# Optimization experiments

Hardware: AMD Instinct MI355X
Metric: run time of the kernel (lower is better)

## Reference

```python
import jax, jax.numpy as jnp
import numpy as np

KNN = 10        # knn init arg
FAC = 2.0       # fac init arg
SIGMA = 0.5     # self.sigma (fixed in module)
N, D = 4096, 128


def setup_inputs() -> dict:
    key = jax.random.key(0)
    k1, k2, k3 = jax.random.split(key, 3)
    return {
        "x": jax.random.normal(k1, (N, D), dtype=jnp.float32),
        "alpha": 0.01 * jax.random.normal(k2, (D,), dtype=jnp.float32),
        "base_noise": jax.random.normal(k3, (D,), dtype=jnp.float32),
    }


def _full_affinity_knn(Xm):
    r = jnp.sum(Xm * Xm, axis=1, keepdims=True)          # [N,1]
    Dx = r - 2.0 * (Xm @ Xm.T) + r.T                     # [N,N]
    # full row sort, take (knn-1)-th smallest distance per row
    sorted_d = jnp.sort(Dx, axis=1)                      # [N,N]
    knn_d = sorted_d[:, KNN - 1]                         # [N]
    # calculate_percentiles(percentile=50)
    s = jnp.sort(knn_d)
    n = s.shape[0]
    idx = int(50.0 / 100.0 * n)
    if n % 2 == 0:
        mu, ml = s[idx], s[idx - 1]
    else:
        mu = ml = s[idx]
    sigma = (mu + ml) / 2.0
    sigma = jnp.where(sigma < 1e-8, jnp.float32(1.0), sigma)
    W = jnp.exp(-Dx / (FAC * sigma))                     # [N,N]
    # Dminus @ W == row-normalize (diag matmul replaced by broadcast divide)
    P = W / jnp.sum(W, axis=1, keepdims=True)
    return P


def reference(x, alpha, base_noise):
    # feature_selector: hard_sigmoid(alpha + sigma*noise) applied per-feature
    z = alpha + SIGMA * base_noise
    gate = jnp.clip(z + 0.5, 0.0, 1.0)
    masked = x * gate[None, :]                           # [N,D]
    P = _full_affinity_knn(masked)                       # [N,N]
    return (P, masked)
```

## Files before the change

### kernel.cpp

```cpp
#include <hip/hip_runtime.h>
#include <math.h>

#define NROW 4096
#define NDIM 128
#define KNN 10
#define LDSS 136

typedef __bf16 bf16x8 __attribute__((ext_vector_type(8)));
typedef unsigned short u16x8 __attribute__((ext_vector_type(8)));
typedef float f32x4 __attribute__((ext_vector_type(4)));

__device__ inline unsigned short f2bf(float f) {
    unsigned int u = __float_as_uint(f);
    u += 0x7FFFu + ((u >> 16) & 1u);
    return (unsigned short)(u >> 16);
}
__device__ inline float bf2f(unsigned short u) {
    return __uint_as_float((unsigned)u << 16);
}


__global__ __launch_bounds__(128) void k_mask(const float* __restrict__ x,
                                              const float* __restrict__ alpha,
                                              const float* __restrict__ noise,
                                              float* __restrict__ masked,
                                              float* __restrict__ r) {
    int row = blockIdx.x;
    int c = threadIdx.x;
    float g = alpha[c] + 0.5f * noise[c] + 0.5f;
    g = fminf(fmaxf(g, 0.0f), 1.0f);
    float m = x[row * NDIM + c] * g;
    masked[row * NDIM + c] = m;
    float v = m * m;
#pragma unroll
    for (int o = 32; o > 0; o >>= 1) v += __shfl_down(v, o, 64);
    __shared__ float partial[2];
    if ((c & 63) == 0) partial[c >> 6] = v;
    __syncthreads();
    if (c == 0) r[row] = partial[0] + partial[1];
}

__global__ __launch_bounds__(256) void k_dx(const float* __restrict__ M,
                                            const float* __restrict__ r,
                                            float* __restrict__ P) {
    __shared__ __align__(16) __bf16 Asm[128 * LDSS];
    __shared__ __align__(16) __bf16 Bsm[128 * LDSS];
    int tid = threadIdx.x;
    int bx = blockIdx.x, by = blockIdx.y;

    {
        const float* Ap = M + (size_t)by * 128 * NDIM;
        const float* Bp = M + (size_t)bx * 128 * NDIM;
        int c = (tid & 15) * 8;
        int r0 = tid >> 4;
#pragma unroll
        for (int i = 0; i < 8; ++i) {
            int row = r0 + i * 16;
            float4 a0 = *(const float4*)(Ap + row * NDIM + c);
            float4 a1 = *(const float4*)(Ap + row * NDIM + c + 4);
            uint4 pa;
            pa.x = (unsigned)f2bf(a0.x) | ((unsigned)f2bf(a0.y) << 16);
            pa.y = (unsigned)f2bf(a0.z) | ((unsigned)f2bf(a0.w) << 16);
            pa.z = (unsigned)f2bf(a1.x) | ((unsigned)f2bf(a1.y) << 16);
            pa.w = (unsigned)f2bf(a1.z) | ((unsigned)f2bf(a1.w) << 16);
            *(uint4*)&Asm[row * LDSS + c] = pa;
            float4 b0 = *(const float4*)(Bp + row * NDIM + c);
            float4 b1 = *(const float4*)(Bp + row * NDIM + c + 4);
            uint4 pb;
            pb.x = (unsigned)f2bf(b0.x) | ((unsigned)f2bf(b0.y) << 16);
            pb.y = (unsigned)f2bf(b0.z) | ((unsigned)f2bf(b0.w) << 16);
            pb.z = (unsigned)f2bf(b1.x) | ((unsigned)f2bf(b1.y) << 16);
            pb.w = (unsigned)f2bf(b1.z) | ((unsigned)f2bf(b1.w) << 16);
            *(uint4*)&Bsm[row * LDSS + c] = pb;
        }
    }
    __syncthreads();

    int wave = tid >> 6, lane = tid & 63;
    int wr = wave >> 1, wc = wave & 1;
    int quad = lane >> 4, l15 = lane & 15;

    f32x4 acc[4][4];
#pragma unroll
    for (int i = 0; i < 4; ++i)
#pragma unroll
        for (int j = 0; j < 4; ++j) acc[i][j] = (f32x4)(0.0f);

#pragma unroll
    for (int kk = 0; kk < 128; kk += 32) {
        int ka = kk + quad * 8;
        bf16x8 af[4], bfr[4];
#pragma unroll
        for (int ti = 0; ti < 4; ++ti)
            af[ti] = *(const bf16x8*)&Asm[(wr * 64 + ti * 16 + l15) * LDSS + ka];
#pragma unroll
        for (int tj = 0; tj < 4; ++tj)
            bfr[tj] = *(const bf16x8*)&Bsm[(wc * 64 + tj * 16 + l15) * LDSS + ka];
#pragma unroll
        for (int ti = 0; ti < 4; ++ti)
#pragma unroll
            for (int tj = 0; tj < 4; ++tj)
                acc[ti][tj] = __builtin_amdgcn_mfma_f32_16x16x32_bf16(
                    af[ti], bfr[tj], acc[ti][tj], 0, 0, 0);
    }

    int gi_base = by * 128 + wr * 64;
    int gj_base = bx * 128 + wc * 64;
    float rrow[4][4], rcol[4];
#pragma unroll
    for (int ti = 0; ti < 4; ++ti)
#pragma unroll
        for (int rg = 0; rg < 4; ++rg)
            rrow[ti][rg] = r[gi_base + ti * 16 + quad * 4 + rg];
#pragma unroll
    for (int tj = 0; tj < 4; ++tj) rcol[tj] = r[gj_base + tj * 16 + l15];
#pragma unroll
    for (int ti = 0; ti < 4; ++ti)
#pragma unroll
        for (int rg = 0; rg < 4; ++rg) {
            int grow = gi_base + ti * 16 + quad * 4 + rg;
            __bf16* brow = (__bf16*)(P + (size_t)grow * NROW + NROW / 2);
#pragma unroll
            for (int tj = 0; tj < 4; ++tj) {
                int gcol = gj_base + tj * 16 + l15;
                float d = rrow[ti][rg] + rcol[tj] - 2.0f * acc[ti][tj][rg];
                ((unsigned short*)brow)[gcol] = f2bf(d);
            }
        }
}

__global__ __launch_bounds__(256) void k_knn(const float* __restrict__ P,
                                             float* __restrict__ knn) {
    int tid = threadIdx.x;
    int wave = tid >> 6, lane = tid & 63;
    int row = blockIdx.x * 4 + wave;
    const unsigned short* drow =
        (const unsigned short*)(P + (size_t)row * NROW + NROW / 2);

    float t[KNN];
#pragma unroll
    for (int j = 0; j < KNN; ++j) t[j] = INFINITY;

#pragma unroll
    for (int c = 0; c < 8; ++c) {
        u16x8 v8 = *(const u16x8*)(drow + (c * 64 + lane) * 8);
#pragma unroll
        for (int e = 0; e < 8; ++e) {
            float cv = bf2f(v8[e]);
#pragma unroll
            for (int j = 0; j < KNN; ++j) {
                float lo = fminf(t[j], cv);
                cv = fmaxf(t[j], cv);
                t[j] = lo;
            }
        }
    }

#pragma unroll
    for (int r = 0; r < KNN; ++r) {
        float v = t[0];
        int src = lane;
#pragma unroll
        for (int o = 1; o < 64; o <<= 1) {
            float ov = __shfl_xor(v, o, 64);
            int osrc = __shfl_xor(src, o, 64);
            if (ov < v || (ov == v && osrc < src)) { v = ov; src = osrc; }
        }
        if (r == KNN - 1) {
            if (lane == 0) knn[row] = v;
        } else if (src == lane) {
#pragma unroll
            for (int j = 0; j < KNN - 1; ++j) t[j] = t[j + 1];
            t[KNN - 1] = INFINITY;
        }
    }
}

__device__ inline unsigned fmap(float f) {
    unsigned b = __float_as_uint(f);
    return b ^ ((b >> 31) ? 0xFFFFFFFFu : 0x80000000u);
}
__device__ inline float funmap(unsigned u) {
    unsigned b = (u & 0x80000000u) ? (u ^ 0x80000000u) : ~u;
    return __uint_as_float(b);
}

__global__ __launch_bounds__(1024) void k_sigma(const float* __restrict__ knn,
                                                float* __restrict__ scale_out) {
    __shared__ unsigned keys[NROW];
    __shared__ unsigned hist[2048];
    __shared__ unsigned s_prefix, s_R;
    __shared__ float red_f[16];
    __shared__ unsigned red_u[16];
    int tid = threadIdx.x;
    if (tid == 0) { s_prefix = 0; s_R = 2047; }
#pragma unroll
    for (int l = 0; l < 4; ++l) keys[tid + l * 1024] = fmap(knn[tid + l * 1024]);
    __syncthreads();

    const int shifts[3] = {21, 10, 0};
    const int widths[3] = {11, 11, 10};
    for (int rd = 0; rd < 3; ++rd) {
        int sh = shifts[rd], w = widths[rd];
        unsigned nb = 1u << w;
        hist[tid] = 0;
        hist[tid + 1024] = 0;
        __syncthreads();
        unsigned prefix = s_prefix;
        unsigned R = s_R;
        int hsh = sh + w;
#pragma unroll
        for (int l = 0; l < 4; ++l) {
            unsigned k = keys[tid + l * 1024];
            bool match = (rd == 0) || ((k >> hsh) == prefix);
            if (match) atomicAdd(&hist[(k >> sh) & (nb - 1u)], 1u);
        }
        __syncthreads();
        if (tid < 64) {
            unsigned chunk = nb >> 6;
            unsigned base = tid * chunk;
            unsigned lsum = 0;
            for (unsigned i = 0; i < chunk; ++i) lsum += hist[base + i];
            unsigned pfx = lsum;
#pragma unroll
            for (int o = 1; o < 64; o <<= 1) {
                unsigned v = __shfl_up(pfx, o, 64);
                if (tid >= o) pfx += v;
            }
            unsigned excl = pfx - lsum;
            if (R >= excl && R < excl + lsum) {
                unsigned cum = excl;
                for (unsigned i = 0; i < chunk; ++i) {
                    unsigned h = hist[base + i];
                    if (R < cum + h) {
                        s_prefix = (prefix << w) | (base + i);
                        s_R = R - cum;
                        break;
                    }
                    cum += h;
                }
            }
        }
        __syncthreads();
    }

    unsigned mlk = s_prefix;
    unsigned cnt = 0, mng = 0xFFFFFFFFu;
#pragma unroll
    for (int l = 0; l < 4; ++l) {
        unsigned k = keys[tid + l * 1024];
        if (k <= mlk) cnt++;
        else mng = min(mng, k);
    }
#pragma unroll
    for (int o = 32; o > 0; o >>= 1) {
        cnt += __shfl_down(cnt, o, 64);
        mng = min(mng, (unsigned)__shfl_down(mng, o, 64));
    }
    int lane = tid & 63, wid = tid >> 6;
    if (lane == 0) { red_u[wid] = cnt; red_f[wid] = __uint_as_float(mng); }
    __syncthreads();
    if (tid == 0) {
        unsigned ctot = 0, m = 0xFFFFFFFFu;
        for (int w = 0; w < 16; ++w) {
            ctot += red_u[w];
            m = min(m, __float_as_uint(red_f[w]));
        }
        float ml = funmap(mlk);
        float mu = (ctot >= 2049u) ? ml : funmap(m);
        float sigma = 0.5f * (mu + ml);
        if (sigma < 1e-8f) sigma = 1.0f;
        scale_out[0] = -1.0f / (2.0f * sigma);
    }
}

__global__ __launch_bounds__(256) void k_norm(float* __restrict__ P,
                                              const float* __restrict__ scale_p) {
    int row = blockIdx.x, tid = threadIdx.x;
    float scale = scale_p[0];
    float* drow = P + (size_t)row * NROW;
    const unsigned short* brow = (const unsigned short*)(drow + NROW / 2);

    u16x8 a = *(const u16x8*)(brow + tid * 16);
    u16x8 b = *(const u16x8*)(brow + tid * 16 + 8);
    float v[16];
#pragma unroll
    for (int e = 0; e < 8; ++e) v[e] = __expf(bf2f(a[e]) * scale);
#pragma unroll
    for (int e = 0; e < 8; ++e) v[8 + e] = __expf(bf2f(b[e]) * scale);
    float sum = 0.0f;
#pragma unroll
    for (int e = 0; e < 16; ++e) sum += v[e];
#pragma unroll
    for (int o = 32; o > 0; o >>= 1) sum += __shfl_down(sum, o, 64);
    __shared__ float ps[4];
    int lane = tid & 63, wid = tid >> 6;
    if (lane == 0) ps[wid] = sum;
    __syncthreads();
    float inv = 1.0f / (ps[0] + ps[1] + ps[2] + ps[3]);
#pragma unroll
    for (int l = 0; l < 4; ++l) {
        float4 o4;
        o4.x = v[l * 4 + 0] * inv;
        o4.y = v[l * 4 + 1] * inv;
        o4.z = v[l * 4 + 2] * inv;
        o4.w = v[l * 4 + 3] * inv;
        *(float4*)(drow + tid * 16 + l * 4) = o4;
    }
}

extern "C" void kernel_launch(void* const* d_in, const int* in_sizes, int n_in,
                              void* d_out, int out_size, void* d_ws, size_t ws_size,
                              hipStream_t stream) {
    const float* x = (const float*)d_in[0];
    const float* alpha = (const float*)d_in[1];
    const float* noise = (const float*)d_in[2];
    float* out = (float*)d_out;
    float* P = out;
    float* masked = out + (size_t)NROW * NROW;
    float* ws = (float*)d_ws;
    float* r = ws;
    float* knn = ws + NROW;
    float* scale = ws + 2 * NROW;

    k_mask<<<NROW, 128, 0, stream>>>(x, alpha, noise, masked, r);
    k_dx<<<dim3(NROW / 128, NROW / 128), 256, 0, stream>>>(masked, r, P);
    k_knn<<<NROW / 4, 256, 0, stream>>>(P, knn);
    k_sigma<<<1, 1024, 0, stream>>>(knn, scale);
    k_norm<<<NROW, 256, 0, stream>>>(P, scale);
}
```

Before: 145.9 us.

## Pre-convert masked rows to bf16 and fold first radix histogram pass into knn

k_mask now also writes a bf16 copy of each masked row into unused scratch space inside the P output. k_dx loads those bf16 rows directly instead of re-reading fp32 data and converting it in every tile. k_knn builds the top-12-bit histogram of the per-row knn distances with global atomics; k_mask zeroes that histogram. This lets the single-block k_sigma skip its first histogram round and keep only two refinement rounds. The gain depends on scratch regions inside P not overlapping, and it adds global atomics to k_knn.

```diff
diff --git a/kernel.cpp b/kernel.cpp
--- a/kernel.cpp
+++ b/kernel.cpp
@@ -18,19 +18,34 @@
 __device__ inline float bf2f(unsigned short u) {
     return __uint_as_float((unsigned)u << 16);
 }
-
+__device__ inline unsigned fmap(float f) {
+    unsigned b = __float_as_uint(f);
+    return b ^ ((b >> 31) ? 0xFFFFFFFFu : 0x80000000u);
+}
+__device__ inline float funmap(unsigned u) {
+    unsigned b = (u & 0x80000000u) ? (u ^ 0x80000000u) : ~u;
+    return __uint_as_float(b);
+}
+
+__device__ inline unsigned short* mb_ptr(float* P, int row) {
+    return (unsigned short*)(P + (size_t)(row >> 5) * NROW) + (row & 31) * NDIM;
+}
 
 __global__ __launch_bounds__(128) void k_mask(const float* __restrict__ x,
                                               const float* __restrict__ alpha,
                                               const float* __restrict__ noise,
                                               float* __restrict__ masked,
-                                              float* __restrict__ r) {
+                                              float* __restrict__ P,
+                                              float* __restrict__ r,
+                                              unsigned* __restrict__ hist) {
     int row = blockIdx.x;
     int c = threadIdx.x;
+    if (c == 0) hist[row] = 0u;
     float g = alpha[c] + 0.5f * noise[c] + 0.5f;
     g = fminf(fmaxf(g, 0.0f), 1.0f);
     float m = x[row * NDIM + c] * g;
     masked[row * NDIM + c] = m;
+    mb_ptr(P, row)[c] = f2bf(m);
     float v = m * m;
 #pragma unroll
     for (int o = 32; o > 0; o >>= 1) v += __shfl_down(v, o, 64);
@@ -40,38 +55,23 @@
     if (c == 0) r[row] = partial[0] + partial[1];
 }
 
-__global__ __launch_bounds__(256) void k_dx(const float* __restrict__ M,
-                                            const float* __restrict__ r,
-                                            float* __restrict__ P) {
+__global__ __launch_bounds__(256) void k_dx(float* __restrict__ P,
+                                            const float* __restrict__ r) {
     __shared__ __align__(16) __bf16 Asm[128 * LDSS];
     __shared__ __align__(16) __bf16 Bsm[128 * LDSS];
     int tid = threadIdx.x;
     int bx = blockIdx.x, by = blockIdx.y;
 
     {
-        const float* Ap = M + (size_t)by * 128 * NDIM;
-        const float* Bp = M + (size_t)bx * 128 * NDIM;
         int c = (tid & 15) * 8;
         int r0 = tid >> 4;
 #pragma unroll
         for (int i = 0; i < 8; ++i) {
             int row = r0 + i * 16;
-            float4 a0 = *(const float4*)(Ap + row * NDIM + c);
-            float4 a1 = *(const float4*)(Ap + row * NDIM + c + 4);
-            uint4 pa;
-            pa.x = (unsigned)f2bf(a0.x) | ((unsigned)f2bf(a0.y) << 16);
-            pa.y = (unsigned)f2bf(a0.z) | ((unsigned)f2bf(a0.w) << 16);
-            pa.z = (unsigned)f2bf(a1.x) | ((unsigned)f2bf(a1.y) << 16);
-            pa.w = (unsigned)f2bf(a1.z) | ((unsigned)f2bf(a1.w) << 16);
-            *(uint4*)&Asm[row * LDSS + c] = pa;
-            float4 b0 = *(const float4*)(Bp + row * NDIM + c);
-            float4 b1 = *(const float4*)(Bp + row * NDIM + c + 4);
-            uint4 pb;
-            pb.x = (unsigned)f2bf(b0.x) | ((unsigned)f2bf(b0.y) << 16);
-            pb.y = (unsigned)f2bf(b0.z) | ((unsigned)f2bf(b0.w) << 16);
-            pb.z = (unsigned)f2bf(b1.x) | ((unsigned)f2bf(b1.y) << 16);
-            pb.w = (unsigned)f2bf(b1.z) | ((unsigned)f2bf(b1.w) << 16);
-            *(uint4*)&Bsm[row * LDSS + c] = pb;
+            *(u16x8*)&Asm[row * LDSS + c] =
+                *(const u16x8*)(mb_ptr(P, by * 128 + row) + c);
+            *(u16x8*)&Bsm[row * LDSS + c] =
+                *(const u16x8*)(mb_ptr(P, bx * 128 + row) + c);
         }
     }
     __syncthreads();
@@ -119,18 +119,20 @@
 #pragma unroll
         for (int rg = 0; rg < 4; ++rg) {
             int grow = gi_base + ti * 16 + quad * 4 + rg;
-            __bf16* brow = (__bf16*)(P + (size_t)grow * NROW + NROW / 2);
+            unsigned short* brow =
+                (unsigned short*)(P + (size_t)grow * NROW + NROW / 2);
 #pragma unroll
             for (int tj = 0; tj < 4; ++tj) {
                 int gcol = gj_base + tj * 16 + l15;
                 float d = rrow[ti][rg] + rcol[tj] - 2.0f * acc[ti][tj][rg];
-                ((unsigned short*)brow)[gcol] = f2bf(d);
+                brow[gcol] = f2bf(d);
             }
         }
 }
 
 __global__ __launch_bounds__(256) void k_knn(const float* __restrict__ P,
-                                             float* __restrict__ knn) {
+                                             float* __restrict__ knn,
+                                             unsigned* __restrict__ hist) {
     int tid = threadIdx.x;
     int wave = tid >> 6, lane = tid & 63;
     int row = blockIdx.x * 4 + wave;
@@ -167,7 +169,10 @@
             if (ov < v || (ov == v && osrc < src)) { v = ov; src = osrc; }
         }
         if (r == KNN - 1) {
-            if (lane == 0) knn[row] = v;
+            if (lane == 0) {
+                knn[row] = v;
+                atomicAdd(&hist[fmap(v) >> 20], 1u);
+            }
         } else if (src == lane) {
 #pragma unroll
             for (int j = 0; j < KNN - 1; ++j) t[j] = t[j + 1];
@@ -176,64 +181,91 @@
     }
 }
 
-__device__ inline unsigned fmap(float f) {
-    unsigned b = __float_as_uint(f);
-    return b ^ ((b >> 31) ? 0xFFFFFFFFu : 0x80000000u);
-}
-__device__ inline float funmap(unsigned u) {
-    unsigned b = (u & 0x80000000u) ? (u ^ 0x80000000u) : ~u;
-    return __uint_as_float(b);
-}
-
 __global__ __launch_bounds__(1024) void k_sigma(const float* __restrict__ knn,
+                                                const unsigned* __restrict__ hist,
                                                 float* __restrict__ scale_out) {
     __shared__ unsigned keys[NROW];
-    __shared__ unsigned hist[2048];
+    __shared__ unsigned h2[1024];
+    __shared__ unsigned wsum[16], woff[16];
     __shared__ unsigned s_prefix, s_R;
     __shared__ float red_f[16];
     __shared__ unsigned red_u[16];
     int tid = threadIdx.x;
-    if (tid == 0) { s_prefix = 0; s_R = 2047; }
+    int lane = tid & 63, wid = tid >> 6;
+
 #pragma unroll
     for (int l = 0; l < 4; ++l) keys[tid + l * 1024] = fmap(knn[tid + l * 1024]);
-    __syncthreads();
-
-    const int shifts[3] = {21, 10, 0};
-    const int widths[3] = {11, 11, 10};
-    for (int rd = 0; rd < 3; ++rd) {
-        int sh = shifts[rd], w = widths[rd];
-        unsigned nb = 1u << w;
-        hist[tid] = 0;
-        hist[tid + 1024] = 0;
+
+    unsigned b[4];
+    unsigned lsum = 0;
+#pragma unroll
+    for (int j = 0; j < 4; ++j) {
+        b[j] = hist[tid * 4 + j];
+        lsum += b[j];
+    }
+    unsigned pfx = lsum;
+#pragma unroll
+    for (int o = 1; o < 64; o <<= 1) {
+        unsigned v = __shfl_up(pfx, o, 64);
+        if (lane >= o) pfx += v;
+    }
+    if (lane == 63) wsum[wid] = pfx;
+    __syncthreads();
+    if (tid == 0) {
+        unsigned acc = 0;
+        for (int i = 0; i < 16; ++i) {
+            woff[i] = acc;
+            acc += wsum[i];
+        }
+    }
+    __syncthreads();
+    unsigned excl = woff[wid] + pfx - lsum;
+    unsigned R0 = 2047;
+    if (R0 >= excl && R0 < excl + lsum) {
+        unsigned cum = excl;
+#pragma unroll
+        for (int j = 0; j < 4; ++j) {
+            if (R0 < cum + b[j]) {
+                s_prefix = tid * 4 + j;
+                s_R = R0 - cum;
+                break;
+            }
+            cum += b[j];
+        }
+    }
+    __syncthreads();
+
+#pragma unroll 1
+    for (int rd = 0; rd < 2; ++rd) {
+        int sh = (rd == 0) ? 10 : 0;
+        h2[tid] = 0;
         __syncthreads();
         unsigned prefix = s_prefix;
         unsigned R = s_R;
-        int hsh = sh + w;
+        int hsh = sh + 10;
 #pragma unroll
         for (int l = 0; l < 4; ++l) {
             unsigned k = keys[tid + l * 1024];
-            bool match = (rd == 0) || ((k >> hsh) == prefix);
-            if (match) atomicAdd(&hist[(k >> sh) & (nb - 1u)], 1u);
+            if ((k >> hsh) == prefix) atomicAdd(&h2[(k >> sh) & 1023u], 1u);
         }
         __syncthreads();
         if (tid < 64) {
-            unsigned chunk = nb >> 6;
-            unsigned base = tid * chunk;
-            unsigned lsum = 0;
-            for (unsigned i = 0; i < chunk; ++i) lsum += hist[base + i];
-            unsigned pfx = lsum;
+            unsigned base = tid * 16;
+            unsigned ls = 0;
+            for (int i = 0; i < 16; ++i) ls += h2[base + i];
+            unsigned p2 = ls;
 #pragma unroll
             for (int o = 1; o < 64; o <<= 1) {
-                unsigned v = __shfl_up(pfx, o, 64);
-                if (tid >= o) pfx += v;
-            }
-            unsigned excl = pfx - lsum;
-            if (R >= excl && R < excl + lsum) {
-                unsigned cum = excl;
-                for (unsigned i = 0; i < chunk; ++i) {
-                    unsigned h = hist[base + i];
+                unsigned v = __shfl_up(p2, o, 64);
+                if (tid >= o) p2 += v;
+            }
+            unsigned ex = p2 - ls;
+            if (R >= ex && R < ex + ls) {
+                unsigned cum = ex;
+                for (int i = 0; i < 16; ++i) {
+                    unsigned h = h2[base + i];
                     if (R < cum + h) {
-                        s_prefix = (prefix << w) | (base + i);
+                        s_prefix = (prefix << 10) | (base + i);
                         s_R = R - cum;
                         break;
                     }
@@ -257,7 +289,6 @@
         cnt += __shfl_down(cnt, o, 64);
         mng = min(mng, (unsigned)__shfl_down(mng, o, 64));
     }
-    int lane = tid & 63, wid = tid >> 6;
     if (lane == 0) { red_u[wid] = cnt; red_f[wid] = __uint_as_float(mng); }
     __syncthreads();
     if (tid == 0) {
@@ -282,12 +313,12 @@
     const unsigned short* brow = (const unsigned short*)(drow + NROW / 2);
 
     u16x8 a = *(const u16x8*)(brow + tid * 16);
-    u16x8 b = *(const u16x8*)(brow + tid * 16 + 8);
+    u16x8 bq = *(const u16x8*)(brow + tid * 16 + 8);
     float v[16];
 #pragma unroll
     for (int e = 0; e < 8; ++e) v[e] = __expf(bf2f(a[e]) * scale);
 #pragma unroll
-    for (int e = 0; e < 8; ++e) v[8 + e] = __expf(bf2f(b[e]) * scale);
+    for (int e = 0; e < 8; ++e) v[8 + e] = __expf(bf2f(bq[e]) * scale);
     float sum = 0.0f;
 #pragma unroll
     for (int e = 0; e < 16; ++e) sum += v[e];
@@ -322,10 +353,11 @@
     float* r = ws;
     float* knn = ws + NROW;
     float* scale = ws + 2 * NROW;
-
-    k_mask<<<NROW, 128, 0, stream>>>(x, alpha, noise, masked, r);
-    k_dx<<<dim3(NROW / 128, NROW / 128), 256, 0, stream>>>(masked, r, P);
-    k_knn<<<NROW / 4, 256, 0, stream>>>(P, knn);
-    k_sigma<<<1, 1024, 0, stream>>>(knn, scale);
+    unsigned* hist = (unsigned*)(ws + 2 * NROW + 128);
+
+    k_mask<<<NROW, 128, 0, stream>>>(x, alpha, noise, masked, P, r, hist);
+    k_dx<<<dim3(NROW / 128, NROW / 128), 256, 0, stream>>>(P, r);
+    k_knn<<<NROW / 4, 256, 0, stream>>>(P, knn, hist);
+    k_sigma<<<1, 1024, 0, stream>>>(knn, hist, scale);
     k_norm<<<NROW, 256, 0, stream>>>(P, scale);
 }
```

New measurement: 180.1 us. 23.4% more time.
